# Performance work log

Measured on AMD Instinct MI355X. Metric: run time of the kernel, lower is better.

Reference implementation:

```python
import jax, jax.numpy as jnp
import numpy as np

D = 1024
H = 16
HD = D // H
SCALE = np.sqrt(HD).astype(np.float32)


def setup_inputs() -> dict:
    key = jax.random.key(0)
    ks = jax.random.split(key, 12)
    s = lambda fan_in: 1.0 / np.sqrt(fan_in)
    return {
        "x": jax.random.normal(ks[0], (4, 2048, D), dtype=jnp.float32),
        "qkv_w": jax.random.uniform(ks[1], (D, 3 * D), jnp.float32, -s(D), s(D)),
        "qkv_b": jax.random.uniform(ks[2], (3 * D,), jnp.float32, -s(D), s(D)),
        "out_w": jax.random.uniform(ks[3], (D, D), jnp.float32, -s(D), s(D)),
        "out_b": jax.random.uniform(ks[4], (D,), jnp.float32, -s(D), s(D)),
        "ln1_g": jnp.ones((D,), jnp.float32),
        "ln1_b": jnp.zeros((D,), jnp.float32),
        "ln2_g": jnp.ones((D,), jnp.float32),
        "ln2_b": jnp.zeros((D,), jnp.float32),
        "ffn_w1": jax.random.uniform(ks[5], (D, 4 * D), jnp.float32, -s(D), s(D)),
        "ffn_b1": jax.random.uniform(ks[6], (4 * D,), jnp.float32, -s(D), s(D)),
        "ffn_w2": jax.random.uniform(ks[7], (4 * D, D), jnp.float32, -s(4 * D), s(4 * D)),
        "ffn_b2": jax.random.uniform(ks[8], (D,), jnp.float32, -s(4 * D), s(4 * D)),
    }


def _layer_norm(x, g, b, eps=1e-5):
    mu = jnp.mean(x, axis=-1, keepdims=True)
    var = jnp.mean(jnp.square(x - mu), axis=-1, keepdims=True)
    return (x - mu) * jax.lax.rsqrt(var + eps) * g + b


def reference(x, qkv_w, qkv_b, out_w, out_b, ln1_g, ln1_b, ln2_g, ln2_b,
              ffn_w1, ffn_b1, ffn_w2, ffn_b2):
    B, L, C = x.shape
    h = _layer_norm(x, ln1_g, ln1_b)
    qkv = (h @ qkv_w + qkv_b).reshape(B, L, 3, H, HD)
    q = jnp.transpose(qkv[:, :, 0], (0, 2, 1, 3))  # [B,H,L,HD]
    k = jnp.transpose(qkv[:, :, 1], (0, 2, 1, 3))
    v = jnp.transpose(qkv[:, :, 2], (0, 2, 1, 3))
    attn = jnp.einsum("bhqd,bhkd->bhqk", q, k) / SCALE
    attn = jax.nn.softmax(attn, axis=-1)
    o = jnp.einsum("bhqk,bhkd->bhqd", attn, v)
    o = jnp.transpose(o, (0, 2, 1, 3)).reshape(B, L, C)
    o = o @ out_w + out_b
    out = _layer_norm(o, ln2_g, ln2_b)
    ffn = jax.nn.gelu(out @ ffn_w1 + ffn_b1, approximate=False) @ ffn_w2 + ffn_b2
    return out + ffn
```

## Files before the change

kernel.cpp:

```cpp
#include <hip/hip_runtime.h>
#include <hip/hip_bf16.h>
#include <math.h>
#include <type_traits>

typedef __bf16 bf16_t;
typedef __bf16 bf16x8 __attribute__((ext_vector_type(8)));
typedef __bf16 bf16x4 __attribute__((ext_vector_type(4)));
typedef float  f32x4  __attribute__((ext_vector_type(4)));
typedef float  f32x16 __attribute__((ext_vector_type(16)));
typedef unsigned int u32x2 __attribute__((ext_vector_type(2)));
typedef unsigned int u32x4 __attribute__((ext_vector_type(4)));

#define MFMA_BF16(a, b, c) __builtin_amdgcn_mfma_f32_16x16x32_bf16(a, b, c, 0, 0, 0)
#define MFMA32_BF16(a, b, c) __builtin_amdgcn_mfma_f32_32x32x16_bf16(a, b, c, 0, 0, 0)

#if __has_builtin(__builtin_amdgcn_exp2f)
__device__ __forceinline__ float fast_exp2(float x) { return __builtin_amdgcn_exp2f(x); }
#else
__device__ __forceinline__ float fast_exp2(float x) { return exp2f(x); }
#endif

__device__ __forceinline__ float fast_gelu(float v) {
  const float u = v * (1.f + 0.044715f * v * v);
  const float tt = fast_exp2(2.3022078f * u);
  return v - v / (tt + 1.f);
}

__device__ __forceinline__ void gload_lds16(const bf16_t* g, bf16_t* l) {
  __builtin_amdgcn_global_load_lds(
      (const __attribute__((address_space(1))) void*)g,
      (__attribute__((address_space(3))) void*)l, 16, 0, 0);
}

__global__ __launch_bounds__(256) void sa_transpose4(const float* __restrict__ s0, bf16_t* __restrict__ d0,
                                                     const float* __restrict__ s1, bf16_t* __restrict__ d1,
                                                     const float* __restrict__ s2, bf16_t* __restrict__ d2,
                                                     const float* __restrict__ s3, bf16_t* __restrict__ d3) {
  __shared__ bf16_t tile[64][65];
  const int bid = blockIdx.x;
  const float* in; bf16_t* out; int K, N, local;
  if (bid < 768)       { in = s0; out = d0; K = 1024; N = 3072; local = bid; }
  else if (bid < 1024) { in = s1; out = d1; K = 1024; N = 1024; local = bid - 768; }
  else if (bid < 2048) { in = s2; out = d2; K = 1024; N = 4096; local = bid - 1024; }
  else                 { in = s3; out = d3; K = 4096; N = 1024; local = bid - 2048; }
  const int nx = N >> 6;
  const int n0 = (local % nx) * 64, k0 = (local / nx) * 64;
  const int t = threadIdx.x;
#pragma unroll
  for (int i = 0; i < 16; ++i) {
    int idx = t + i * 256;
    int r = idx >> 6, c = idx & 63;
    tile[r][c] = (bf16_t)in[(size_t)(k0 + r) * N + n0 + c];
  }
  __syncthreads();
#pragma unroll
  for (int i = 0; i < 16; ++i) {
    int idx = t + i * 256;
    int r = idx >> 6, c = idx & 63;
    out[(size_t)(n0 + r) * K + k0 + c] = tile[c][r];
  }
}

__global__ __launch_bounds__(256) void sa_layernorm(const float* __restrict__ in,
                                                    const float* __restrict__ gamma,
                                                    const float* __restrict__ beta,
                                                    bf16_t* __restrict__ out_bf) {
  const int row = blockIdx.x, t = threadIdx.x;
  const float4 v = *(const float4*)(in + (size_t)row * 1024 + t * 4);
  float s  = v.x + v.y + v.z + v.w;
  float ss = v.x * v.x + v.y * v.y + v.z * v.z + v.w * v.w;
#pragma unroll
  for (int m = 1; m < 64; m <<= 1) {
    s  += __shfl_xor(s, m, 64);
    ss += __shfl_xor(ss, m, 64);
  }
  __shared__ float red[8];
  const int w = t >> 6, lane = t & 63;
  if (lane == 0) { red[w] = s; red[4 + w] = ss; }
  __syncthreads();
  s  = red[0] + red[1] + red[2] + red[3];
  ss = red[4] + red[5] + red[6] + red[7];
  const float mu   = s * (1.f / 1024.f);
  const float rstd = rsqrtf(ss * (1.f / 1024.f) - mu * mu + 1e-5f);
  const float4 gv = *(const float4*)(gamma + t * 4);
  const float4 bv = *(const float4*)(beta + t * 4);
  bf16x4 ob = { (bf16_t)((v.x - mu) * rstd * gv.x + bv.x),
                (bf16_t)((v.y - mu) * rstd * gv.y + bv.y),
                (bf16_t)((v.z - mu) * rstd * gv.z + bv.z),
                (bf16_t)((v.w - mu) * rstd * gv.w + bv.w) };
  *(bf16x4*)(out_bf + (size_t)row * 1024 + t * 4) = ob;
}

__global__ __launch_bounds__(256) void sa_layernorm_b(const bf16_t* __restrict__ in,
                                                      const float* __restrict__ gamma,
                                                      const float* __restrict__ beta,
                                                      bf16_t* __restrict__ out_bf) {
  const int row = blockIdx.x, t = threadIdx.x;
  const bf16x4 iv = *(const bf16x4*)(in + (size_t)row * 1024 + t * 4);
  const float v0 = (float)iv[0], v1 = (float)iv[1], v2 = (float)iv[2], v3 = (float)iv[3];
  float s  = v0 + v1 + v2 + v3;
  float ss = v0 * v0 + v1 * v1 + v2 * v2 + v3 * v3;
#pragma unroll
  for (int m = 1; m < 64; m <<= 1) {
    s  += __shfl_xor(s, m, 64);
    ss += __shfl_xor(ss, m, 64);
  }
  __shared__ float red[8];
  const int w = t >> 6, lane = t & 63;
  if (lane == 0) { red[w] = s; red[4 + w] = ss; }
  __syncthreads();
  s  = red[0] + red[1] + red[2] + red[3];
  ss = red[4] + red[5] + red[6] + red[7];
  const float mu   = s * (1.f / 1024.f);
  const float rstd = rsqrtf(ss * (1.f / 1024.f) - mu * mu + 1e-5f);
  const float4 gv = *(const float4*)(gamma + t * 4);
  const float4 bv = *(const float4*)(beta + t * 4);
  bf16x4 ob = { (bf16_t)((v0 - mu) * rstd * gv.x + bv.x),
                (bf16_t)((v1 - mu) * rstd * gv.y + bv.y),
                (bf16_t)((v2 - mu) * rstd * gv.z + bv.z),
                (bf16_t)((v3 - mu) * rstd * gv.w + bv.w) };
  *(bf16x4*)(out_bf + (size_t)row * 1024 + t * 4) = ob;
}

template <int EPI>
__global__ __launch_bounds__(256, 2) void sa_gemm4(const bf16_t* __restrict__ A,
                                                   const bf16_t* __restrict__ Bt,
                                                   const float* __restrict__ bias,
                                                   int K, int N,
                                                   float* __restrict__ fout,
                                                   bf16_t* __restrict__ bfout,
                                                   const bf16_t* __restrict__ res,
                                                   bf16_t* __restrict__ qb,
                                                   bf16_t* __restrict__ kb,
                                                   bf16_t* __restrict__ vb) {
  __shared__ __attribute__((aligned(16))) bf16_t As[2][128][64];
  __shared__ __attribute__((aligned(16))) bf16_t Bs[2][128][64];

  const int gx = gridDim.x;
  const int flat = blockIdx.y * gx + blockIdx.x;
  const int c = flat & 7;
  const int local = flat >> 3;
  const int sg = local >> 6;
  const int rem = local & 63;
  const int by = c * 8 + (rem >> 3);
  const int bx = sg * 8 + (rem & 7);

  const int m0 = by * 128, n0 = bx * 128;
  const int t = threadIdx.x;
  const int w = t >> 6, lane = t & 63;
  const int wr = w >> 1, wc = w & 1;
  const int fr = lane & 15, fq = lane >> 4;
  const int swz = fr & 7;
  const int srow = lane >> 3;
  const int scol = ((lane & 7) ^ srow) * 8;
  const int NT = K >> 6;

  const f32x4 fzero = { 0.f, 0.f, 0.f, 0.f };
  f32x4 acc[4][4];
#pragma unroll
  for (int mi = 0; mi < 4; ++mi)
#pragma unroll
    for (int ni = 0; ni < 4; ++ni) acc[mi][ni] = fzero;

  auto stage = [&](int tt, int sb) {
#pragma unroll
    for (int i = 0; i < 4; ++i) {
      const int ch = w * 4 + i;
      const int row = ch * 8 + srow;
      gload_lds16(A  + (size_t)(m0 + row) * K + tt * 64 + scol, &As[sb][ch * 8][0]);
      gload_lds16(Bt + (size_t)(n0 + row) * K + tt * 64 + scol, &Bs[sb][ch * 8][0]);
    }
  };

  auto compute = [&](auto curc) {
    constexpr int cur = decltype(curc)::value;
    bf16x8 af[4][2], bfr[4][2];
#pragma unroll
    for (int mi = 0; mi < 4; ++mi)
#pragma unroll
      for (int kk = 0; kk < 2; ++kk)
        af[mi][kk] = *(const bf16x8*)&As[cur][wr * 64 + mi * 16 + fr][((kk * 4 + fq) ^ swz) * 8];
#pragma unroll
    for (int ni = 0; ni < 4; ++ni)
#pragma unroll
      for (int kk = 0; kk < 2; ++kk)
        bfr[ni][kk] = *(const bf16x8*)&Bs[cur][wc * 64 + ni * 16 + fr][((kk * 4 + fq) ^ swz) * 8];
    __builtin_amdgcn_s_setprio(1);
#pragma unroll
    for (int kk = 0; kk < 2; ++kk)
#pragma unroll
      for (int mi = 0; mi < 4; ++mi)
#pragma unroll
        for (int ni = 0; ni < 4; ++ni)
          acc[mi][ni] = MFMA_BF16(af[mi][kk], bfr[ni][kk], acc[mi][ni]);
    __builtin_amdgcn_s_setprio(0);
  };

  stage(0, 0);
  __syncthreads();

  for (int tt = 0; tt < NT; tt += 2) {
    stage(tt + 1, 1);
    compute(std::integral_constant<int, 0>{});
    __syncthreads();
    if (tt + 2 < NT) stage(tt + 2, 0);
    compute(std::integral_constant<int, 1>{});
    __syncthreads();
  }

#pragma unroll
  for (int ni = 0; ni < 4; ++ni) {
    const int n = n0 + wc * 64 + ni * 16 + fr;
    const float bn = bias[n];
#pragma unroll
    for (int mi = 0; mi < 4; ++mi) {
      const int mbase = m0 + wr * 64 + mi * 16 + fq * 4;
      float vv[4];
#pragma unroll
      for (int r = 0; r < 4; ++r) vv[r] = acc[mi][ni][r] + bn;
      if constexpr (EPI == 0) {
        const int which = n >> 10;
        const int hh = (n >> 6) & 15;
        const int d = n & 63;
        const int b = mbase >> 11, l = mbase & 2047;
        if (which == 0) {
#pragma unroll
          for (int r = 0; r < 4; ++r)
            qb[((size_t)(b * 16 + hh) * 2048 + l + r) * 64 + d] =
                (bf16_t)(vv[r] * (0.125f * 1.44269504088896340736f));
        } else if (which == 1) {
#pragma unroll
          for (int r = 0; r < 4; ++r)
            kb[((size_t)(b * 16 + hh) * 2048 + l + r) * 64 + d] = (bf16_t)vv[r];
        } else {
          bf16x4 pv = { (bf16_t)vv[0], (bf16_t)vv[1], (bf16_t)vv[2], (bf16_t)vv[3] };
          *(bf16x4*)(vb + ((size_t)(b * 16 + hh) * 64 + d) * 2048 + l) = pv;
        }
      } else if constexpr (EPI == 1) {
#pragma unroll
        for (int r = 0; r < 4; ++r)
          bfout[(size_t)(mbase + r) * N + n] = (bf16_t)vv[r];
      } else if constexpr (EPI == 2) {
#pragma unroll
        for (int r = 0; r < 4; ++r)
          bfout[(size_t)(mbase + r) * N + n] = (bf16_t)fast_gelu(vv[r]);
      } else {
#pragma unroll
        for (int r = 0; r < 4; ++r)
          fout[(size_t)(mbase + r) * N + n] = vv[r] + (float)res[(size_t)(mbase + r) * N + n];
      }
    }
  }
}

__global__ __launch_bounds__(256) void sa_attn32(const bf16_t* __restrict__ qb,
                                                 const bf16_t* __restrict__ kb,
                                                 const bf16_t* __restrict__ vb,
                                                 bf16_t* __restrict__ out) {
  __shared__ __attribute__((aligned(16))) bf16_t Ks[2][64][64];
  __shared__ __attribute__((aligned(16))) bf16_t Vt[2][64][64];

  const int nwg = gridDim.x * gridDim.y;
  const int flat = blockIdx.y * gridDim.x + blockIdx.x;
  const int wg = (flat & 7) * (nwg >> 3) + (flat >> 3);
  const int qblk = wg & 15, bh = wg >> 4;

  const int t = threadIdx.x, wq = t >> 6, lane = t & 63;
  const int q31 = lane & 31, hi = lane >> 5;
  const int qx = q31 & 7;
  const size_t base = (size_t)bh * 2048 * 64;

  const int srow = lane >> 3;
  const int sunit = (lane & 7) ^ srow;

  const bf16_t* qrow = qb + base + (size_t)(qblk * 128 + wq * 32 + q31) * 64 + hi * 8;
  bf16x8 qf[4];
#pragma unroll
  for (int c = 0; c < 4; ++c) qf[c] = *(const bf16x8*)(qrow + c * 16);

  auto STAGE = [&](int kv0, int buf) {
#pragma unroll
    for (int i = 0; i < 2; ++i) {
      const int rb = wq * 16 + i * 8;
      gload_lds16(kb + base + (size_t)(kv0 + rb + srow) * 64 + sunit * 8,
                  &Ks[buf][rb][0]);
      gload_lds16(vb + base + (size_t)(rb + srow) * 2048 + kv0 + sunit * 8,
                  &Vt[buf][rb][0]);
    }
  };

  f32x16 o0, o1, la0, la1;
#pragma unroll
  for (int i = 0; i < 16; ++i) { o0[i] = 0.f; o1[i] = 0.f; la0[i] = 0.f; la1[i] = 0.f; }

  auto COMPUTE = [&](auto bufc) {
    constexpr int buf = decltype(bufc)::value;
    f32x16 s0, s1;
#pragma unroll
    for (int i = 0; i < 16; ++i) { s0[i] = 0.f; s1[i] = 0.f; }
    __builtin_amdgcn_s_setprio(1);
#pragma unroll
    for (int c = 0; c < 4; ++c) {
      bf16x8 ka0 = *(const bf16x8*)&Ks[buf][q31]     [((2 * c + hi) ^ qx) * 8];
      bf16x8 ka1 = *(const bf16x8*)&Ks[buf][q31 + 32][((2 * c + hi) ^ qx) * 8];
      s0 = MFMA32_BF16(ka0, qf[c], s0);
      s1 = MFMA32_BF16(ka1, qf[c], s1);
    }
    __builtin_amdgcn_s_setprio(0);

#pragma unroll
    for (int i = 0; i < 16; ++i) s0[i] = fast_exp2(s0[i]);
#pragma unroll
    for (int i = 0; i < 16; ++i) s1[i] = fast_exp2(s1[i]);
    la0 += s0;
    la1 += s1;

    u32x4 pw[4];
#define PACK_CHUNK(c, SB, off)                                                      \
    {                                                                               \
      unsigned int x0, x1, y0, y1;                                                  \
      asm("v_cvt_pk_bf16_f32 %0, %1, %2" : "=v"(x0) : "v"(SB[off+0]), "v"(SB[off+1])); \
      asm("v_cvt_pk_bf16_f32 %0, %1, %2" : "=v"(x1) : "v"(SB[off+2]), "v"(SB[off+3])); \
      asm("v_cvt_pk_bf16_f32 %0, %1, %2" : "=v"(y0) : "v"(SB[off+4]), "v"(SB[off+5])); \
      asm("v_cvt_pk_bf16_f32 %0, %1, %2" : "=v"(y1) : "v"(SB[off+6]), "v"(SB[off+7])); \
      u32x2 r0 = __builtin_amdgcn_permlane32_swap(x0, y0, false, false);            \
      u32x2 r1 = __builtin_amdgcn_permlane32_swap(x1, y1, false, false);            \
      pw[c][0] = r0[0]; pw[c][1] = r1[0]; pw[c][2] = r0[1]; pw[c][3] = r1[1];       \
    }
    PACK_CHUNK(0, s0, 0)
    PACK_CHUNK(1, s0, 8)
    PACK_CHUNK(2, s1, 0)
    PACK_CHUNK(3, s1, 8)
#undef PACK_CHUNK

    __builtin_amdgcn_s_setprio(1);
#pragma unroll
    for (int c = 0; c < 4; ++c) {
      bf16x8 pf = *(const bf16x8*)&pw[c];
      bf16x8 va0 = *(const bf16x8*)&Vt[buf][q31]     [((2 * c + hi) ^ qx) * 8];
      bf16x8 va1 = *(const bf16x8*)&Vt[buf][q31 + 32][((2 * c + hi) ^ qx) * 8];
      o0 = MFMA32_BF16(va0, pf, o0);
      o1 = MFMA32_BF16(va1, pf, o1);
    }
    __builtin_amdgcn_s_setprio(0);
  };

  STAGE(0, 0);
  __syncthreads();

  for (int it = 0; it < 32; it += 2) {
    STAGE((it + 1) * 64, 1);
    COMPUTE(std::integral_constant<int, 0>{});
    __syncthreads();
    if (it + 2 < 32) STAGE((it + 2) * 64, 0);
    COMPUTE(std::integral_constant<int, 1>{});
    __syncthreads();
  }

  f32x16 lt = la0 + la1;
  float lsum;
  {
    float p0 = (lt[0] + lt[1]) + (lt[2] + lt[3]);
    float p1 = (lt[4] + lt[5]) + (lt[6] + lt[7]);
    float p2 = (lt[8] + lt[9]) + (lt[10] + lt[11]);
    float p3 = (lt[12] + lt[13]) + (lt[14] + lt[15]);
    lsum = (p0 + p1) + (p2 + p3);
  }
  lsum += __shfl_xor(lsum, 32, 64);
  const float linv = 1.f / lsum;
  const int b = bh >> 4, h = bh & 15;
  const int qg = qblk * 128 + wq * 32 + q31;
  bf16_t* orow = out + (size_t)(b * 2048 + qg) * 1024 + h * 64;
#pragma unroll
  for (int rg = 0; rg < 4; ++rg) {
    bf16x4 olo = { (bf16_t)(o0[4 * rg + 0] * linv), (bf16_t)(o0[4 * rg + 1] * linv),
                   (bf16_t)(o0[4 * rg + 2] * linv), (bf16_t)(o0[4 * rg + 3] * linv) };
    *(bf16x4*)(orow + 8 * rg + 4 * hi) = olo;
    bf16x4 ohi = { (bf16_t)(o1[4 * rg + 0] * linv), (bf16_t)(o1[4 * rg + 1] * linv),
                   (bf16_t)(o1[4 * rg + 2] * linv), (bf16_t)(o1[4 * rg + 3] * linv) };
    *(bf16x4*)(orow + 32 + 8 * rg + 4 * hi) = ohi;
  }
}

extern "C" void kernel_launch(void* const* d_in, const int* in_sizes, int n_in,
                              void* d_out, int out_size, void* d_ws, size_t ws_size,
                              hipStream_t stream) {
  const float* x      = (const float*)d_in[0];
  const float* qkv_w  = (const float*)d_in[1];
  const float* qkv_b  = (const float*)d_in[2];
  const float* out_w  = (const float*)d_in[3];
  const float* out_b  = (const float*)d_in[4];
  const float* ln1_g  = (const float*)d_in[5];
  const float* ln1_b  = (const float*)d_in[6];
  const float* ln2_g  = (const float*)d_in[7];
  const float* ln2_b  = (const float*)d_in[8];
  const float* ffn_w1 = (const float*)d_in[9];
  const float* ffn_b1 = (const float*)d_in[10];
  const float* ffn_w2 = (const float*)d_in[11];
  const float* ffn_b2 = (const float*)d_in[12];
  float* outp = (float*)d_out;

  char* p = (char*)d_ws;
  auto alloc = [&](size_t bytes) { char* r = p; p += bytes; return r; };
  bf16_t* qkvw_t = (bf16_t*)alloc((size_t)3072 * 1024 * 2);
  bf16_t* outw_t = (bf16_t*)alloc((size_t)1024 * 1024 * 2);
  bf16_t* w1_t   = (bf16_t*)alloc((size_t)4096 * 1024 * 2);
  bf16_t* w2_t   = (bf16_t*)alloc((size_t)1024 * 4096 * 2);
  bf16_t* h_bf   = (bf16_t*)alloc((size_t)8192 * 1024 * 2);
  bf16_t* q_buf  = (bf16_t*)alloc((size_t)8192 * 1024 * 2);
  bf16_t* k_buf  = (bf16_t*)alloc((size_t)8192 * 1024 * 2);
  bf16_t* v_buf  = (bf16_t*)alloc((size_t)8192 * 1024 * 2);
  bf16_t* a_bf   = (bf16_t*)alloc((size_t)8192 * 1024 * 2);
  bf16_t* o_bf   = (bf16_t*)alloc((size_t)8192 * 1024 * 2);
  bf16_t* out_bf = (bf16_t*)alloc((size_t)8192 * 1024 * 2);
  bf16_t* t_bf   = (bf16_t*)alloc((size_t)8192 * 4096 * 2);

  sa_transpose4<<<3072, 256, 0, stream>>>(qkv_w, qkvw_t, out_w, outw_t,
                                          ffn_w1, w1_t, ffn_w2, w2_t);

  sa_layernorm<<<8192, 256, 0, stream>>>(x, ln1_g, ln1_b, h_bf);

  sa_gemm4<0><<<dim3(3072 / 128, 8192 / 128), 256, 0, stream>>>(
      h_bf, qkvw_t, qkv_b, 1024, 3072, nullptr, nullptr, nullptr, q_buf, k_buf, v_buf);

  sa_attn32<<<dim3(16, 64), 256, 0, stream>>>(q_buf, k_buf, v_buf, a_bf);

  sa_gemm4<1><<<dim3(1024 / 128, 8192 / 128), 256, 0, stream>>>(
      a_bf, outw_t, out_b, 1024, 1024, nullptr, o_bf, nullptr, nullptr, nullptr, nullptr);

  sa_layernorm_b<<<8192, 256, 0, stream>>>(o_bf, ln2_g, ln2_b, out_bf);

  sa_gemm4<2><<<dim3(4096 / 128, 8192 / 128), 256, 0, stream>>>(
      out_bf, w1_t, ffn_b1, 1024, 4096, nullptr, t_bf, nullptr, nullptr, nullptr, nullptr);

  sa_gemm4<3><<<dim3(1024 / 128, 8192 / 128), 256, 0, stream>>>(
      t_bf, w2_t, ffn_b2, 4096, 1024, outp, nullptr, out_bf, nullptr, nullptr, nullptr);
}
```

Baseline: 364.5 us.

## Load GEMM A fragments directly from global memory, keep only B in LDS

The GEMM kernel no longer stages the A tile through shared memory. Each wave reads its A MFMA fragments directly from global memory into registers, while B keeps the double-buffered async LDS staging. This halves LDS usage and raises launch bounds to three blocks per CU to increase occupancy. The trade-off is unhidden global-load latency on A right before the MFMAs, duplicated A reads across the two wave columns, and tighter register limits.

Measured after the change: 547.3 us. +50.1%, slower.

```diff
diff --git a/kernel.cpp b/kernel.cpp
--- a/kernel.cpp
+++ b/kernel.cpp
@@ -123,7 +123,7 @@
 }
 
 template <int EPI>
-__global__ __launch_bounds__(256, 2) void sa_gemm4(const bf16_t* __restrict__ A,
+__global__ __launch_bounds__(256, 3) void sa_gemm6(const bf16_t* __restrict__ A,
                                                    const bf16_t* __restrict__ Bt,
                                                    const float* __restrict__ bias,
                                                    int K, int N,
@@ -133,7 +133,6 @@
                                                    bf16_t* __restrict__ qb,
                                                    bf16_t* __restrict__ kb,
                                                    bf16_t* __restrict__ vb) {
-  __shared__ __attribute__((aligned(16))) bf16_t As[2][128][64];
   __shared__ __attribute__((aligned(16))) bf16_t Bs[2][128][64];
 
   const int gx = gridDim.x;
@@ -162,24 +161,28 @@
 #pragma unroll
     for (int ni = 0; ni < 4; ++ni) acc[mi][ni] = fzero;
 
-  auto stage = [&](int tt, int sb) {
+  const bf16_t* arow[4];
+#pragma unroll
+  for (int mi = 0; mi < 4; ++mi)
+    arow[mi] = A + (size_t)(m0 + wr * 64 + mi * 16 + fr) * K + fq * 8;
+
+  auto stageB = [&](int tt, int sb) {
 #pragma unroll
     for (int i = 0; i < 4; ++i) {
       const int ch = w * 4 + i;
       const int row = ch * 8 + srow;
-      gload_lds16(A  + (size_t)(m0 + row) * K + tt * 64 + scol, &As[sb][ch * 8][0]);
       gload_lds16(Bt + (size_t)(n0 + row) * K + tt * 64 + scol, &Bs[sb][ch * 8][0]);
     }
   };
 
-  auto compute = [&](auto curc) {
+  auto compute = [&](auto curc, int tt) {
     constexpr int cur = decltype(curc)::value;
     bf16x8 af[4][2], bfr[4][2];
 #pragma unroll
     for (int mi = 0; mi < 4; ++mi)
 #pragma unroll
       for (int kk = 0; kk < 2; ++kk)
-        af[mi][kk] = *(const bf16x8*)&As[cur][wr * 64 + mi * 16 + fr][((kk * 4 + fq) ^ swz) * 8];
+        af[mi][kk] = *(const bf16x8*)(arow[mi] + tt * 64 + kk * 32);
 #pragma unroll
     for (int ni = 0; ni < 4; ++ni)
 #pragma unroll
@@ -196,15 +199,15 @@
     __builtin_amdgcn_s_setprio(0);
   };
 
-  stage(0, 0);
+  stageB(0, 0);
   __syncthreads();
 
   for (int tt = 0; tt < NT; tt += 2) {
-    stage(tt + 1, 1);
-    compute(std::integral_constant<int, 0>{});
+    stageB(tt + 1, 1);
+    compute(std::integral_constant<int, 0>{}, tt);
     __syncthreads();
-    if (tt + 2 < NT) stage(tt + 2, 0);
-    compute(std::integral_constant<int, 1>{});
+    if (tt + 2 < NT) stageB(tt + 2, 0);
+    compute(std::integral_constant<int, 1>{}, tt + 1);
     __syncthreads();
   }
 
@@ -420,19 +423,19 @@
 
   sa_layernorm<<<8192, 256, 0, stream>>>(x, ln1_g, ln1_b, h_bf);
 
-  sa_gemm4<0><<<dim3(3072 / 128, 8192 / 128), 256, 0, stream>>>(
+  sa_gemm6<0><<<dim3(3072 / 128, 8192 / 128), 256, 0, stream>>>(
       h_bf, qkvw_t, qkv_b, 1024, 3072, nullptr, nullptr, nullptr, q_buf, k_buf, v_buf);
 
   sa_attn32<<<dim3(16, 64), 256, 0, stream>>>(q_buf, k_buf, v_buf, a_bf);
 
-  sa_gemm4<1><<<dim3(1024 / 128, 8192 / 128), 256, 0, stream>>>(
+  sa_gemm6<1><<<dim3(1024 / 128, 8192 / 128), 256, 0, stream>>>(
       a_bf, outw_t, out_b, 1024, 1024, nullptr, o_bf, nullptr, nullptr, nullptr, nullptr);
 
   sa_layernorm_b<<<8192, 256, 0, stream>>>(o_bf, ln2_g, ln2_b, out_bf);
 
-  sa_gemm4<2><<<dim3(4096 / 128, 8192 / 128), 256, 0, stream>>>(
+  sa_gemm6<2><<<dim3(4096 / 128, 8192 / 128), 256, 0, stream>>>(
       out_bf, w1_t, ffn_b1, 1024, 4096, nullptr, t_bf, nullptr, nullptr, nullptr, nullptr);
 
-  sa_gemm4<3><<<dim3(1024 / 128, 8192 / 128), 256, 0, stream>>>(
+  sa_gemm6<3><<<dim3(1024 / 128, 8192 / 128), 256, 0, stream>>>(
       t_bf, w2_t, ffn_b2, 4096, 1024, outp, nullptr, out_bf, nullptr, nullptr, nullptr);
 }
```
